# Kernel optimization log

Measured on AMD Instinct MI355X. Metric: run time of the kernel, lower is better.

The kernel has to match this reference:

```python
import jax, jax.numpy as jnp
import numpy as np

B, S, D, H = 4, 2048, 1024, 16
DK = D // H

def setup_inputs() -> dict:
    key = jax.random.key(0)
    k1, k2, k3 = jax.random.split(key, 3)
    x = jax.random.normal(k1, (B, S, D), dtype=jnp.float32)
    # kaiming-uniform-ish scale for (d_k, d_model) fan_in = d_model
    bound = 1.0 / np.sqrt(D)
    w_qkv = jax.random.uniform(k2, (3, H, DK, D), dtype=jnp.float32, minval=-bound, maxval=bound)
    w_o = jax.random.uniform(k3, (D, D), dtype=jnp.float32, minval=-bound, maxval=bound)
    return {"x": x, "w_qkv": w_qkv, "w_o": w_o}

def reference(x, w_qkv, w_o):
    seq_len = x.shape[-2]
    d_k = w_qkv.shape[-2]
    # qkv projection: (b s m),(qkv h k m) -> (qkv b h s k)
    qkv = jnp.einsum('bsm,qhkm->qbhsk', x, w_qkv)
    Q, K, V = qkv[0], qkv[1], qkv[2]
    scores = jnp.einsum('bhqk,bhsk->bhqs', Q, K) / jnp.sqrt(jnp.float32(d_k))
    causal = jnp.triu(jnp.ones((seq_len, seq_len), dtype=bool), k=1)
    scores = jnp.where(causal, -jnp.inf, scores)
    probs = jax.nn.softmax(scores, axis=-1)  # (b h s s)
    attn = jnp.einsum('bhqs,bhsk->bhqk', probs, V)
    # concat heads: (b h s k) -> (b s h*k)
    attn = jnp.transpose(attn, (0, 2, 1, 3)).reshape(x.shape[0], seq_len, -1)
    # out proj: y = attn @ w_o.T
    return jnp.einsum('bsd,md->bsm', attn, w_o)
```

## Files before the change

kernel.cpp:

```cpp
#include <hip/hip_runtime.h>
#include <stdint.h>
#include <stddef.h>

typedef unsigned short u16;
typedef float  f32x4  __attribute__((ext_vector_type(4)));
typedef short  s16x8  __attribute__((ext_vector_type(8)));
typedef short  s16x4  __attribute__((ext_vector_type(4)));
typedef __bf16 bf16x8 __attribute__((ext_vector_type(8)));
typedef __bf16 bf16x4 __attribute__((ext_vector_type(4)));
typedef u16    u16x4  __attribute__((ext_vector_type(4)));

#define DEV static __device__ __forceinline__

DEV u16 f2bf(float f){
  uint32_t u = __builtin_bit_cast(uint32_t, f);
  u += 0x7FFFu + ((u >> 16) & 1u);
  return (u16)(u >> 16);
}

DEV f32x4 mfma16(s16x8 a, s16x8 b, f32x4 c){
  return __builtin_amdgcn_mfma_f32_16x16x32_bf16(
      __builtin_bit_cast(bf16x8, a), __builtin_bit_cast(bf16x8, b), c, 0, 0, 0);
}

DEV f32x4 mfma16k(s16x4 a, s16x4 b, f32x4 c){
  return __builtin_amdgcn_mfma_f32_16x16x16bf16_1k(a, b, c, 0, 0, 0);
}

DEV float exp2_fast(float x){ return __builtin_exp2f(x); }

DEV void gl_lds16(const u16* g, u16* l){
  __builtin_amdgcn_global_load_lds(
      (__attribute__((address_space(1))) void*)(g),
      (__attribute__((address_space(3))) void*)(l), 16, 0, 0);
}

__global__ __launch_bounds__(256) void cvt_all(const float* __restrict__ x,
                                               const float* __restrict__ wqkv,
                                               const float* __restrict__ wo,
                                               u16* __restrict__ outb){
  const int N1 = 2097152;
  const int N2 = N1 + 786432;
  const int NT = N2 + 262144;
  const int stride = gridDim.x * blockDim.x;
  for (int i = blockIdx.x * blockDim.x + threadIdx.x; i < NT; i += stride){
    const float* src; int j;
    if (i < N1){ src = x; j = i; }
    else if (i < N2){ src = wqkv; j = i - N1; }
    else { src = wo; j = i - N2; }
    float4 v = *(const float4*)(src + (size_t)j * 4);
    u16x4 o = { f2bf(v.x), f2bf(v.y), f2bf(v.z), f2bf(v.w) };
    *(u16x4*)(outb + (size_t)i * 4) = o;
  }
}

DEV void gemm_core(const u16* __restrict__ A, const u16* __restrict__ Bw,
                   int K, int bm, int bn, u16* ldsA, u16* ldsB, f32x4 acc[4][4])
{
  const int lane = threadIdx.x & 63;
  const int wave = threadIdx.x >> 6;
  const int wm = (wave >> 1) * 64, wn = (wave & 1) * 64;
  const int l8 = (lane & 7) * 8;
  const int lr = lane >> 3;
  const int fr = lane & 15;
  const int k8 = (lane >> 4) * 8;

  #pragma unroll
  for (int m = 0; m < 4; m++)
    #pragma unroll
    for (int n = 0; n < 4; n++){ f32x4 z = {0.f,0.f,0.f,0.f}; acc[m][n] = z; }

  const int nkt = K >> 6;
  for (int kt = 0; kt < nkt; ++kt){
    const int kb = kt * 64;
    #pragma unroll
    for (int i = 0; i < 4; i++){
      const int c   = wave * 4 + i;
      const int row = c * 8 + lr;
      gl_lds16(A  + (size_t)(bm + row) * K + kb + l8, ldsA + c * 512);
      gl_lds16(Bw + (size_t)(bn + row) * K + kb + l8, ldsB + c * 512);
    }
    __syncthreads();
    #pragma unroll
    for (int kk = 0; kk < 2; ++kk){
      s16x8 af[4], bfr[4];
      #pragma unroll
      for (int m = 0; m < 4; m++) af[m]  = *(const s16x8*)(ldsA + (wm + m*16 + fr)*64 + kk*32 + k8);
      #pragma unroll
      for (int n = 0; n < 4; n++) bfr[n] = *(const s16x8*)(ldsB + (wn + n*16 + fr)*64 + kk*32 + k8);
      #pragma unroll
      for (int m = 0; m < 4; m++)
        #pragma unroll
        for (int n = 0; n < 4; n++)
          acc[m][n] = mfma16(af[m], bfr[n], acc[m][n]);
    }
    __syncthreads();
  }
}

__global__ __launch_bounds__(256) void gemm_qkv(const u16* __restrict__ xb,
                                                const u16* __restrict__ wb,
                                                u16* __restrict__ Qd,
                                                u16* __restrict__ Kd,
                                                u16* __restrict__ Vtd)
{
  __shared__ __align__(16) u16 ldsA[128*64];
  __shared__ __align__(16) u16 ldsB[128*64];
  f32x4 acc[4][4];
  const int bm = blockIdx.x * 128, bn = blockIdx.y * 128;
  gemm_core(xb, wb, 1024, bm, bn, ldsA, ldsB, acc);

  const int lane = threadIdx.x & 63, wave = threadIdx.x >> 6;
  const int wm = (wave >> 1) * 64, wn = (wave & 1) * 64;
  const int fr = lane & 15, r4 = (lane >> 4) * 4;
  const int q = bn >> 10;

  #pragma unroll
  for (int m = 0; m < 4; m++){
    const int i0 = bm + wm + m*16 + r4;
    const int b  = i0 >> 11;
    const int s0 = i0 & 2047;
    #pragma unroll
    for (int n = 0; n < 4; n++){
      const int ng = bn + wn + n*16 + fr;
      const int h  = (ng >> 6) & 15, kd = ng & 63;
      const size_t bh = (size_t)(b * 16 + h);
      if (q == 0){
        #pragma unroll
        for (int r = 0; r < 4; r++)
          Qd[(bh*2048 + s0 + r)*64 + kd] = f2bf(acc[m][n][r] * 0.18033688011112042f);
      } else if (q == 1){
        #pragma unroll
        for (int r = 0; r < 4; r++)
          Kd[(bh*2048 + s0 + r)*64 + kd] = f2bf(acc[m][n][r]);
      } else {
        u16x4 v = { f2bf(acc[m][n][0]), f2bf(acc[m][n][1]),
                    f2bf(acc[m][n][2]), f2bf(acc[m][n][3]) };
        *(u16x4*)(Vtd + (bh*64 + kd)*2048 + s0) = v;
      }
    }
  }
}

__global__ __launch_bounds__(256) void gemm_outp(const u16* __restrict__ attnb,
                                                 const u16* __restrict__ wob,
                                                 float* __restrict__ C)
{
  __shared__ __align__(16) u16 ldsA[128*64];
  __shared__ __align__(16) u16 ldsB[128*64];
  f32x4 acc[4][4];
  const int bm = blockIdx.x * 128, bn = blockIdx.y * 128;
  gemm_core(attnb, wob, 1024, bm, bn, ldsA, ldsB, acc);

  const int lane = threadIdx.x & 63, wave = threadIdx.x >> 6;
  const int wm = (wave >> 1) * 64, wn = (wave & 1) * 64;
  const int fr = lane & 15, r4 = (lane >> 4) * 4;
  #pragma unroll
  for (int m = 0; m < 4; m++){
    const int i0 = bm + wm + m*16 + r4;
    #pragma unroll
    for (int n = 0; n < 4; n++){
      const int ng = bn + wn + n*16 + fr;
      #pragma unroll
      for (int r = 0; r < 4; r++)
        C[(size_t)(i0 + r) * 1024 + ng] = acc[m][n][r];
    }
  }
}

DEV void chunk_step(const u16* Kc, const u16* Vc, int kb, int q0c,
                    const s16x8 (&qfc)[2][2], f32x4 (&Oc)[2][4],
                    float* m2, float* l2,
                    int fr, int g, int f, int r4)
{
  f32x4 sc[2][4];
  #pragma unroll
  for (int rg = 0; rg < 2; rg++)
    #pragma unroll
    for (int mi = 0; mi < 4; mi++){ f32x4 z = {0.f,0.f,0.f,0.f}; sc[rg][mi] = z; }
  __builtin_amdgcn_s_setprio(1);
  #pragma unroll
  for (int kk = 0; kk < 2; kk++)
    #pragma unroll
    for (int mi = 0; mi < 4; mi++){
      s16x8 kf = *(const s16x8*)(Kc + (mi*16 + fr)*64 + ((kk*4 + g) ^ f)*8);
      sc[0][mi] = mfma16(kf, qfc[0][kk], sc[0][mi]);
      sc[1][mi] = mfma16(kf, qfc[1][kk], sc[1][mi]);
    }
  __builtin_amdgcn_s_setprio(0);

  s16x4 pb[2][4];
  #pragma unroll
  for (int rg = 0; rg < 2; rg++){
    const int q_g = q0c + rg*16 + fr;
    float tmax = -1e30f;
    if (kb + 63 > q0c + rg*16){
      #pragma unroll
      for (int mi = 0; mi < 4; mi++)
        #pragma unroll
        for (int r = 0; r < 4; r++){
          const int s_g = kb + mi*16 + r4 + r;
          float v = sc[rg][mi][r];
          v = (s_g > q_g) ? -1e30f : v;
          sc[rg][mi][r] = v;
          tmax = fmaxf(tmax, v);
        }
    } else {
      #pragma unroll
      for (int mi = 0; mi < 4; mi++)
        #pragma unroll
        for (int r = 0; r < 4; r++)
          tmax = fmaxf(tmax, sc[rg][mi][r]);
    }
    float m_new = m2[rg];
    if (!__all(tmax <= m_new + 8.f)){
      float tm = fmaxf(tmax, __shfl_xor(tmax, 16));
      tm = fmaxf(tm, __shfl_xor(tm, 32));
      m_new = fmaxf(m_new, tm);
      const float corr = exp2_fast(m2[rg] - m_new);
      m2[rg] = m_new;
      l2[rg] *= corr;
      #pragma unroll
      for (int n = 0; n < 4; n++)
        #pragma unroll
        for (int r = 0; r < 4; r++)
          Oc[rg][n][r] *= corr;
    }
    float tsum = 0.f;
    #pragma unroll
    for (int mi = 0; mi < 4; mi++){
      f32x4 e;
      #pragma unroll
      for (int r = 0; r < 4; r++){
        e[r] = exp2_fast(sc[rg][mi][r] - m_new);
        tsum += e[r];
      }
      pb[rg][mi] = __builtin_bit_cast(s16x4, __builtin_convertvector(e, bf16x4));
    }
    l2[rg] += tsum;
  }

  __builtin_amdgcn_s_setprio(1);
  #pragma unroll
  for (int mi = 0; mi < 4; mi++){
    #pragma unroll
    for (int n = 0; n < 4; n++){
      s16x4 vf = *(const s16x4*)(Vc + (n*16 + fr)*64 + ((2*mi + (g >> 1)) ^ f)*8 + (g & 1)*4);
      Oc[0][n] = mfma16k(vf, pb[0][mi], Oc[0][n]);
      Oc[1][n] = mfma16k(vf, pb[1][mi], Oc[1][n]);
    }
  }
  __builtin_amdgcn_s_setprio(0);
}

__global__ __launch_bounds__(256, 2) void attn_fwd(const u16* __restrict__ Qd,
                                                   const u16* __restrict__ Kd,
                                                   const u16* __restrict__ Vtd,
                                                   u16* __restrict__ attnb)
{
  __shared__ __align__(16) u16 Kl[2][64*64];
  __shared__ __align__(16) u16 Vl[2][64*64];

  const int t = threadIdx.x;
  const int lane = t & 63, w = t >> 6;
  const int wg = blockIdx.x;
  const int bh = 8 * (wg & 7) + (wg >> 6);
  const int p  = (wg >> 3) & 7;
  const int qh = 8 + p, ql = 7 - p;
  const u16* Qp = Qd  + (size_t)bh * 2048 * 64;
  const u16* Kp = Kd  + (size_t)bh * 2048 * 64;
  const u16* Vp = Vtd + (size_t)bh * 64 * 2048;

  const int fr = lane & 15, g = lane >> 4;
  const int f  = fr & 7;
  const int k8 = g * 8, r4 = g * 4;
  const int qh0 = qh * 128 + w * 32;
  const int ql0 = ql * 128 + w * 32;
  const int nkt = 2 * qh + 2;

  s16x8 qfh[2][2], qfl[2][2];
  #pragma unroll
  for (int rg = 0; rg < 2; rg++)
    #pragma unroll
    for (int kk = 0; kk < 2; kk++){
      qfh[rg][kk] = *(const s16x8*)(Qp + (size_t)(qh0 + rg*16 + fr) * 64 + kk*32 + k8);
      qfl[rg][kk] = *(const s16x8*)(Qp + (size_t)(ql0 + rg*16 + fr) * 64 + kk*32 + k8);
    }

  f32x4 Oh[2][4], Ol[2][4];
  #pragma unroll
  for (int rg = 0; rg < 2; rg++)
    #pragma unroll
    for (int n = 0; n < 4; n++){
      f32x4 z = {0.f,0.f,0.f,0.f}; Oh[rg][n] = z; Ol[rg][n] = z;
    }
  float mh[2] = {-1e30f, -1e30f}, lh[2] = {0.f, 0.f};
  float ml[2] = {-1e30f, -1e30f}, ll[2] = {0.f, 0.f};

  #pragma unroll
  for (int i = 0; i < 2; i++){
    const int L = i*256 + t;
    const int row = L >> 3, c = L & 7;
    const int cs = c ^ (row & 7);
    gl_lds16(Kp + (size_t)row * 64 + cs*8,   Kl[0] + L*8);
    gl_lds16(Vp + (size_t)row * 2048 + cs*8, Vl[0] + L*8);
  }

  for (int kt = 0; kt < nkt; ++kt){
    __syncthreads();
    const int cur = kt & 1;
    if (kt + 1 < nkt){
      const int kb2 = (kt + 1) * 64;
      u16* Kn = Kl[cur ^ 1]; u16* Vn = Vl[cur ^ 1];
      #pragma unroll
      for (int i = 0; i < 2; i++){
        const int L = i*256 + t;
        const int row = L >> 3, c = L & 7;
        const int cs = c ^ (row & 7);
        gl_lds16(Kp + (size_t)(kb2 + row) * 64 + cs*8, Kn + L*8);
        gl_lds16(Vp + (size_t)row * 2048 + kb2 + cs*8, Vn + L*8);
      }
    }
    const int kb = kt * 64;
    const u16* Kc = Kl[cur];
    const u16* Vc = Vl[cur];

    if (kb <= qh0 + 31)
      chunk_step(Kc, Vc, kb, qh0, qfh, Oh, mh, lh, fr, g, f, r4);
    if (kb <= ql0 + 31)
      chunk_step(Kc, Vc, kb, ql0, qfl, Ol, ml, ll, fr, g, f, r4);
  }

  const int b = bh >> 4, h = bh & 15;
  #pragma unroll
  for (int rg = 0; rg < 2; rg++){
    float lsh = lh[rg];
    lsh += __shfl_xor(lsh, 16);
    lsh += __shfl_xor(lsh, 32);
    float lsl = ll[rg];
    lsl += __shfl_xor(lsl, 16);
    lsl += __shfl_xor(lsl, 32);
    const float invh = 1.0f / lsh;
    const float invl = 1.0f / lsl;
    const int sh = qh0 + rg*16 + fr;
    const int sl = ql0 + rg*16 + fr;
    #pragma unroll
    for (int n = 0; n < 4; n++){
      u16x4 vh = { f2bf(Oh[rg][n][0]*invh), f2bf(Oh[rg][n][1]*invh),
                   f2bf(Oh[rg][n][2]*invh), f2bf(Oh[rg][n][3]*invh) };
      *(u16x4*)(attnb + (((size_t)b*2048 + sh)*16 + h)*64 + n*16 + r4) = vh;
      u16x4 vl = { f2bf(Ol[rg][n][0]*invl), f2bf(Ol[rg][n][1]*invl),
                   f2bf(Ol[rg][n][2]*invl), f2bf(Ol[rg][n][3]*invl) };
      *(u16x4*)(attnb + (((size_t)b*2048 + sl)*16 + h)*64 + n*16 + r4) = vl;
    }
  }
}

extern "C" void kernel_launch(void* const* d_in, const int* in_sizes, int n_in,
                              void* d_out, int out_size, void* d_ws, size_t ws_size,
                              hipStream_t stream)
{
  const float* x    = (const float*)d_in[0];
  const float* wqkv = (const float*)d_in[1];
  const float* wo   = (const float*)d_in[2];
  float* out = (float*)d_out;

  char* ws = (char*)d_ws;
  u16* xb    = (u16*)(ws);
  u16* wqb   = (u16*)(ws + 16777216);
  u16* wob   = (u16*)(ws + 23068672);
  u16* Qd    = (u16*)(ws + 25165824);
  u16* Kd    = (u16*)(ws + 41943040);
  u16* Vtd   = (u16*)(ws + 58720256);
  u16* attnb = xb;

  cvt_all<<<3072, 256, 0, stream>>>(x, wqkv, wo, xb);
  gemm_qkv<<<dim3(64, 24), 256, 0, stream>>>(xb, wqb, Qd, Kd, Vtd);
  attn_fwd<<<dim3(512), 256, 0, stream>>>(Qd, Kd, Vtd, attnb);
  gemm_outp<<<dim3(64, 8), 256, 0, stream>>>(attnb, wob, out);
}
```

Baseline: 211.6 us.

## Split attention query tiles across twice as many workgroups with MFMA row sums

Each wave now handles one 16-row query group per high/low tile instead of two, so the grid doubles to 1024 workgroups and launch bounds allow 4 blocks per CU. The intent is more occupancy and better latency hiding in the attention kernel. The softmax row sum moves from scalar adds plus cross-lane shuffles to an extra MFMA against a ones vector. The K/V staging address math is also simplified with precomputed pointers. In exchange, each K/V tile is loaded twice as often across workgroups, and per-wave MFMA work per loaded tile is halved.

```diff
diff --git a/kernel.cpp b/kernel.cpp
--- a/kernel.cpp
+++ b/kernel.cpp
@@ -168,92 +168,82 @@
   }
 }
 
-DEV void chunk_step(const u16* Kc, const u16* Vc, int kb, int q0c,
-                    const s16x8 (&qfc)[2][2], f32x4 (&Oc)[2][4],
-                    float* m2, float* l2,
-                    int fr, int g, int f, int r4)
-{
-  f32x4 sc[2][4];
-  #pragma unroll
-  for (int rg = 0; rg < 2; rg++)
-    #pragma unroll
-    for (int mi = 0; mi < 4; mi++){ f32x4 z = {0.f,0.f,0.f,0.f}; sc[rg][mi] = z; }
+DEV void chunk_step1(const u16* Kc, const u16* Vc, int kb, int q0,
+                     const s16x8 (&qf)[2], f32x4 (&O)[4], f32x4 &L,
+                     float &mrun, s16x4 ones,
+                     int fr, int g, int f, int r4)
+{
+  f32x4 sc[4];
+  #pragma unroll
+  for (int mi = 0; mi < 4; mi++){ f32x4 z = {0.f,0.f,0.f,0.f}; sc[mi] = z; }
   __builtin_amdgcn_s_setprio(1);
   #pragma unroll
   for (int kk = 0; kk < 2; kk++)
     #pragma unroll
     for (int mi = 0; mi < 4; mi++){
       s16x8 kf = *(const s16x8*)(Kc + (mi*16 + fr)*64 + ((kk*4 + g) ^ f)*8);
-      sc[0][mi] = mfma16(kf, qfc[0][kk], sc[0][mi]);
-      sc[1][mi] = mfma16(kf, qfc[1][kk], sc[1][mi]);
+      sc[mi] = mfma16(kf, qf[kk], sc[mi]);
     }
   __builtin_amdgcn_s_setprio(0);
 
-  s16x4 pb[2][4];
-  #pragma unroll
-  for (int rg = 0; rg < 2; rg++){
-    const int q_g = q0c + rg*16 + fr;
-    float tmax = -1e30f;
-    if (kb + 63 > q0c + rg*16){
-      #pragma unroll
-      for (int mi = 0; mi < 4; mi++)
-        #pragma unroll
-        for (int r = 0; r < 4; r++){
-          const int s_g = kb + mi*16 + r4 + r;
-          float v = sc[rg][mi][r];
-          v = (s_g > q_g) ? -1e30f : v;
-          sc[rg][mi][r] = v;
-          tmax = fmaxf(tmax, v);
-        }
-    } else {
-      #pragma unroll
-      for (int mi = 0; mi < 4; mi++)
-        #pragma unroll
-        for (int r = 0; r < 4; r++)
-          tmax = fmaxf(tmax, sc[rg][mi][r]);
-    }
-    float m_new = m2[rg];
-    if (!__all(tmax <= m_new + 8.f)){
-      float tm = fmaxf(tmax, __shfl_xor(tmax, 16));
-      tm = fmaxf(tm, __shfl_xor(tm, 32));
-      m_new = fmaxf(m_new, tm);
-      const float corr = exp2_fast(m2[rg] - m_new);
-      m2[rg] = m_new;
-      l2[rg] *= corr;
-      #pragma unroll
-      for (int n = 0; n < 4; n++)
-        #pragma unroll
-        for (int r = 0; r < 4; r++)
-          Oc[rg][n][r] *= corr;
-    }
-    float tsum = 0.f;
-    #pragma unroll
-    for (int mi = 0; mi < 4; mi++){
-      f32x4 e;
+  const int q_g = q0 + fr;
+  float tmax = -1e30f;
+  if (kb + 63 > q0){
+    #pragma unroll
+    for (int mi = 0; mi < 4; mi++)
       #pragma unroll
       for (int r = 0; r < 4; r++){
-        e[r] = exp2_fast(sc[rg][mi][r] - m_new);
-        tsum += e[r];
+        const int s_g = kb + mi*16 + r4 + r;
+        float v = sc[mi][r];
+        v = (s_g > q_g) ? -1e30f : v;
+        sc[mi][r] = v;
+        tmax = fmaxf(tmax, v);
       }
-      pb[rg][mi] = __builtin_bit_cast(s16x4, __builtin_convertvector(e, bf16x4));
-    }
-    l2[rg] += tsum;
+  } else {
+    #pragma unroll
+    for (int mi = 0; mi < 4; mi++)
+      #pragma unroll
+      for (int r = 0; r < 4; r++)
+        tmax = fmaxf(tmax, sc[mi][r]);
+  }
+  float m_new = mrun;
+  if (!__all(tmax <= m_new + 8.f)){
+    float tm = fmaxf(tmax, __shfl_xor(tmax, 16));
+    tm = fmaxf(tm, __shfl_xor(tm, 32));
+    m_new = fmaxf(m_new, tm);
+    const float corr = exp2_fast(mrun - m_new);
+    mrun = m_new;
+    L[0] *= corr;
+    #pragma unroll
+    for (int n = 0; n < 4; n++)
+      #pragma unroll
+      for (int r = 0; r < 4; r++)
+        O[n][r] *= corr;
+  }
+  s16x4 pb[4];
+  #pragma unroll
+  for (int mi = 0; mi < 4; mi++){
+    f32x4 e;
+    #pragma unroll
+    for (int r = 0; r < 4; r++)
+      e[r] = exp2_fast(sc[mi][r] - m_new);
+    pb[mi] = __builtin_bit_cast(s16x4, __builtin_convertvector(e, bf16x4));
   }
 
   __builtin_amdgcn_s_setprio(1);
   #pragma unroll
   for (int mi = 0; mi < 4; mi++){
+    L = mfma16k(ones, pb[mi], L);
     #pragma unroll
     for (int n = 0; n < 4; n++){
       s16x4 vf = *(const s16x4*)(Vc + (n*16 + fr)*64 + ((2*mi + (g >> 1)) ^ f)*8 + (g & 1)*4);
-      Oc[0][n] = mfma16k(vf, pb[0][mi], Oc[0][n]);
-      Oc[1][n] = mfma16k(vf, pb[1][mi], Oc[1][n]);
+      O[n] = mfma16k(vf, pb[mi], O[n]);
     }
   }
   __builtin_amdgcn_s_setprio(0);
 }
 
-__global__ __launch_bounds__(256, 2) void attn_fwd(const u16* __restrict__ Qd,
+__global__ __launch_bounds__(256, 4) void attn_fwd(const u16* __restrict__ Qd,
                                                    const u16* __restrict__ Kd,
                                                    const u16* __restrict__ Vtd,
                                                    u16* __restrict__ attnb)
@@ -264,8 +254,9 @@
   const int t = threadIdx.x;
   const int lane = t & 63, w = t >> 6;
   const int wg = blockIdx.x;
-  const int bh = 8 * (wg & 7) + (wg >> 6);
-  const int p  = (wg >> 3) & 7;
+  const int bh = 8 * (wg & 7) + (wg >> 7);
+  const int ph = (wg >> 3) & 15;
+  const int p  = ph >> 1, half = ph & 1;
   const int qh = 8 + p, ql = 7 - p;
   const u16* Qp = Qd  + (size_t)bh * 2048 * 64;
   const u16* Kp = Kd  + (size_t)bh * 2048 * 64;
@@ -274,85 +265,75 @@
   const int fr = lane & 15, g = lane >> 4;
   const int f  = fr & 7;
   const int k8 = g * 8, r4 = g * 4;
-  const int qh0 = qh * 128 + w * 32;
-  const int ql0 = ql * 128 + w * 32;
+  const int rgs = half * 4 + w;
+  const int qh0 = qh * 128 + rgs * 16;
+  const int ql0 = ql * 128 + rgs * 16;
   const int nkt = 2 * qh + 2;
 
-  s16x8 qfh[2][2], qfl[2][2];
-  #pragma unroll
-  for (int rg = 0; rg < 2; rg++)
-    #pragma unroll
-    for (int kk = 0; kk < 2; kk++){
-      qfh[rg][kk] = *(const s16x8*)(Qp + (size_t)(qh0 + rg*16 + fr) * 64 + kk*32 + k8);
-      qfl[rg][kk] = *(const s16x8*)(Qp + (size_t)(ql0 + rg*16 + fr) * 64 + kk*32 + k8);
-    }
-
-  f32x4 Oh[2][4], Ol[2][4];
-  #pragma unroll
-  for (int rg = 0; rg < 2; rg++)
-    #pragma unroll
-    for (int n = 0; n < 4; n++){
-      f32x4 z = {0.f,0.f,0.f,0.f}; Oh[rg][n] = z; Ol[rg][n] = z;
-    }
-  float mh[2] = {-1e30f, -1e30f}, lh[2] = {0.f, 0.f};
-  float ml[2] = {-1e30f, -1e30f}, ll[2] = {0.f, 0.f};
-
-  #pragma unroll
-  for (int i = 0; i < 2; i++){
-    const int L = i*256 + t;
-    const int row = L >> 3, c = L & 7;
-    const int cs = c ^ (row & 7);
-    gl_lds16(Kp + (size_t)row * 64 + cs*8,   Kl[0] + L*8);
-    gl_lds16(Vp + (size_t)row * 2048 + cs*8, Vl[0] + L*8);
-  }
+  const s16x4 ones = { 0x3F80, 0x3F80, 0x3F80, 0x3F80 };
+
+  s16x8 qfh[2], qfl[2];
+  #pragma unroll
+  for (int kk = 0; kk < 2; kk++){
+    qfh[kk] = *(const s16x8*)(Qp + (size_t)(qh0 + fr) * 64 + kk*32 + k8);
+    qfl[kk] = *(const s16x8*)(Qp + (size_t)(ql0 + fr) * 64 + kk*32 + k8);
+  }
+
+  f32x4 Ohi[4], Olo[4], Lhi, Llo;
+  #pragma unroll
+  for (int n = 0; n < 4; n++){
+    f32x4 z = {0.f,0.f,0.f,0.f}; Ohi[n] = z; Olo[n] = z;
+  }
+  { f32x4 z = {0.f,0.f,0.f,0.f}; Lhi = z; Llo = z; }
+  float mh = -1e30f, ml = -1e30f;
+
+  const int Lr  = t >> 3;
+  const int cs8 = ((t & 7) ^ (Lr & 7)) * 8;
+  const u16* kS = Kp + Lr * 64 + cs8;
+  const u16* vS = Vp + (size_t)Lr * 2048 + cs8;
+
+  gl_lds16(kS,         (u16*)Kl + t*8);
+  gl_lds16(kS + 2048,  (u16*)Kl + t*8 + 2048);
+  gl_lds16(vS,         (u16*)Vl + t*8);
+  gl_lds16(vS + 65536, (u16*)Vl + t*8 + 2048);
+  kS += 4096; vS += 64;
 
   for (int kt = 0; kt < nkt; ++kt){
     __syncthreads();
     const int cur = kt & 1;
     if (kt + 1 < nkt){
-      const int kb2 = (kt + 1) * 64;
-      u16* Kn = Kl[cur ^ 1]; u16* Vn = Vl[cur ^ 1];
-      #pragma unroll
-      for (int i = 0; i < 2; i++){
-        const int L = i*256 + t;
-        const int row = L >> 3, c = L & 7;
-        const int cs = c ^ (row & 7);
-        gl_lds16(Kp + (size_t)(kb2 + row) * 64 + cs*8, Kn + L*8);
-        gl_lds16(Vp + (size_t)row * 2048 + kb2 + cs*8, Vn + L*8);
-      }
-    }
+      u16* kD = (u16*)Kl + (cur ^ 1) * 4096 + t*8;
+      u16* vD = (u16*)Vl + (cur ^ 1) * 4096 + t*8;
+      gl_lds16(kS,         kD);
+      gl_lds16(kS + 2048,  kD + 2048);
+      gl_lds16(vS,         vD);
+      gl_lds16(vS + 65536, vD + 2048);
+    }
+    kS += 4096; vS += 64;
+
     const int kb = kt * 64;
     const u16* Kc = Kl[cur];
     const u16* Vc = Vl[cur];
 
-    if (kb <= qh0 + 31)
-      chunk_step(Kc, Vc, kb, qh0, qfh, Oh, mh, lh, fr, g, f, r4);
-    if (kb <= ql0 + 31)
-      chunk_step(Kc, Vc, kb, ql0, qfl, Ol, ml, ll, fr, g, f, r4);
+    if (kb <= qh0 + 15)
+      chunk_step1(Kc, Vc, kb, qh0, qfh, Ohi, Lhi, mh, ones, fr, g, f, r4);
+    if (kb <= ql0 + 15)
+      chunk_step1(Kc, Vc, kb, ql0, qfl, Olo, Llo, ml, ones, fr, g, f, r4);
   }
 
   const int b = bh >> 4, h = bh & 15;
-  #pragma unroll
-  for (int rg = 0; rg < 2; rg++){
-    float lsh = lh[rg];
-    lsh += __shfl_xor(lsh, 16);
-    lsh += __shfl_xor(lsh, 32);
-    float lsl = ll[rg];
-    lsl += __shfl_xor(lsl, 16);
-    lsl += __shfl_xor(lsl, 32);
-    const float invh = 1.0f / lsh;
-    const float invl = 1.0f / lsl;
-    const int sh = qh0 + rg*16 + fr;
-    const int sl = ql0 + rg*16 + fr;
-    #pragma unroll
-    for (int n = 0; n < 4; n++){
-      u16x4 vh = { f2bf(Oh[rg][n][0]*invh), f2bf(Oh[rg][n][1]*invh),
-                   f2bf(Oh[rg][n][2]*invh), f2bf(Oh[rg][n][3]*invh) };
-      *(u16x4*)(attnb + (((size_t)b*2048 + sh)*16 + h)*64 + n*16 + r4) = vh;
-      u16x4 vl = { f2bf(Ol[rg][n][0]*invl), f2bf(Ol[rg][n][1]*invl),
-                   f2bf(Ol[rg][n][2]*invl), f2bf(Ol[rg][n][3]*invl) };
-      *(u16x4*)(attnb + (((size_t)b*2048 + sl)*16 + h)*64 + n*16 + r4) = vl;
-    }
+  const float invh = 1.0f / Lhi[0];
+  const float invl = 1.0f / Llo[0];
+  const int sh = qh0 + fr;
+  const int sl = ql0 + fr;
+  #pragma unroll
+  for (int n = 0; n < 4; n++){
+    u16x4 vh = { f2bf(Ohi[n][0]*invh), f2bf(Ohi[n][1]*invh),
+                 f2bf(Ohi[n][2]*invh), f2bf(Ohi[n][3]*invh) };
+    *(u16x4*)(attnb + (((size_t)b*2048 + sh)*16 + h)*64 + n*16 + r4) = vh;
+    u16x4 vl = { f2bf(Olo[n][0]*invl), f2bf(Olo[n][1]*invl),
+                 f2bf(Olo[n][2]*invl), f2bf(Olo[n][3]*invl) };
+    *(u16x4*)(attnb + (((size_t)b*2048 + sl)*16 + h)*64 + n*16 + r4) = vl;
   }
 }
 
@@ -376,6 +357,6 @@
 
   cvt_all<<<3072, 256, 0, stream>>>(x, wqkv, wo, xb);
   gemm_qkv<<<dim3(64, 24), 256, 0, stream>>>(xb, wqb, Qd, Kd, Vtd);
-  attn_fwd<<<dim3(512), 256, 0, stream>>>(Qd, Kd, Vtd, attnb);
+  attn_fwd<<<dim3(1024), 256, 0, stream>>>(Qd, Kd, Vtd, attnb);
   gemm_outp<<<dim3(64, 8), 256, 0, stream>>>(attnb, wob, out);
 }
```

Result: faster. 200.3 us (-5.4%).
